# Performance work log

Measured on AMD Instinct MI355X. Metric: run time of the kernel, lower is better.

## Reference

```python
import jax, jax.numpy as jnp
from jax import lax
import numpy as np

T, N, E = 8, 20000, 640000
D_IN, H, K = 2, 64, 3


def setup_inputs() -> dict:
    key = jax.random.key(0)
    ks = jax.random.split(key, 10)
    x = jax.random.normal(ks[0], (T, N, D_IN), dtype=jnp.float32)
    edge_idx = jax.random.randint(ks[1], (T, 2, E), 0, N, dtype=jnp.int64)
    edge_attr = jax.random.uniform(ks[2], (T, E), dtype=jnp.float32)
    Fin = D_IN + H
    s = 0.05
    Wr = jax.random.normal(ks[3], (K, Fin, H), dtype=jnp.float32) * s
    Wu = jax.random.normal(ks[4], (K, Fin, H), dtype=jnp.float32) * s
    Wc = jax.random.normal(ks[5], (K, Fin, H), dtype=jnp.float32) * s
    br = jnp.zeros((H,), dtype=jnp.float32)
    bu = jnp.zeros((H,), dtype=jnp.float32)
    bc = jnp.zeros((H,), dtype=jnp.float32)
    return {"x": x, "edge_idx": edge_idx, "edge_attr": edge_attr,
            "Wr": Wr, "br": br, "Wu": Wu, "bu": bu, "Wc": Wc, "bc": bc}


def reference(x, edge_idx, edge_attr, Wr, br, Wu, bu, Wc, bc):
    n = x.shape[1]
    k_hops = Wr.shape[0]

    def cheb(v, src, dst, wn, W, b):
        # Chebyshev recursion on scaled Laplacian (PyG ChebConv, lambda_max=2)
        def prop(t):
            return jax.ops.segment_sum(wn[:, None] * t[src], dst, num_segments=n)
        Tx0 = v
        out = Tx0 @ W[0]
        Tx1 = prop(Tx0)
        out = out + Tx1 @ W[1]
        for kk in range(2, k_hops):
            Tx2 = 2.0 * prop(Tx1) - Tx0
            out = out + Tx2 @ W[kk]
            Tx0, Tx1 = Tx1, Tx2
        return out + b

    def step(h, inp):
        x_t, ei, w_t = inp
        src, dst = ei[0], ei[1]
        # sym-normalized Laplacian, scaled by 2/lambda_max=1; self-loop weight is 0
        deg = jax.ops.segment_sum(w_t, src, num_segments=n)
        safe = jnp.where(deg > 0, deg, 1.0)
        dinv = jnp.where(deg > 0, lax.rsqrt(safe), 0.0)
        wn = -dinv[src] * w_t * dinv[dst]
        comb = jnp.concatenate([x_t, h], axis=1)
        r = jax.nn.sigmoid(cheb(comb, src, dst, wn, Wr, br))
        u = jax.nn.sigmoid(cheb(comb, src, dst, wn, Wu, bu))
        c = jnp.tanh(cheb(jnp.concatenate([x_t, r * h], axis=1), src, dst, wn, Wc, bc))
        h_new = u * h + (1.0 - u) * c
        return h_new, None

    h0 = jnp.zeros((n, br.shape[0]), dtype=x.dtype)
    h_final, _ = lax.scan(step, h0, (x, edge_idx, edge_attr))
    return h_final
```

## Files before the change

kernel.cpp:

```cpp
#include <hip/hip_runtime.h>

#define NN 20000
#define EE 640000
#define TT 8
#define HF 64
#define AS 232
#define ACS 104
#define BSS 194
#define PBLK 5000
#define TILE 2560
#define NBIN 250
#define BWID 80
#define ECAP 3072
#define LCAP 24

typedef _Float16 f16;
typedef unsigned int uint;
typedef unsigned char uchar;
typedef __attribute__((ext_vector_type(8))) _Float16 half8;
typedef __attribute__((ext_vector_type(4))) float floatx4;
typedef __attribute__((ext_vector_type(4))) uint uint4v;

__device__ __forceinline__ float lo16f(uint v) { return (float)__builtin_bit_cast(f16, (unsigned short)(v & 0xffff)); }
__device__ __forceinline__ float hi16f(uint v) { return (float)__builtin_bit_cast(f16, (unsigned short)(v >> 16)); }
__device__ __forceinline__ uint pk16(float a, float b) {
    unsigned short ua = __builtin_bit_cast(unsigned short, (f16)a);
    unsigned short ub = __builtin_bit_cast(unsigned short, (f16)b);
    return (uint)ua | ((uint)ub << 16);
}

__global__ __launch_bounds__(256) void k_prepW(
    const float* __restrict__ Wr, const float* __restrict__ Wu, const float* __restrict__ Wc,
    f16* __restrict__ Wp, f16* __restrict__ Wcp)
{
    int idx = blockIdx.x * 256 + threadIdx.x;
    if (idx < 8 * 7 * 64) {
        int lane = idx & 63;
        int kb = (idx >> 6) % 7;
        int nb = (idx >> 6) / 7;
        int col = nb * 16 + (lane & 15);
        int g = col >> 6, jj = col & 63;
        const float* W = (g == 0) ? Wr : Wu;
        half8 v;
        #pragma unroll
        for (int e = 0; e < 8; e++) {
            int k = kb * 32 + ((lane >> 4) << 3) + e;
            float val = 0.f;
            if (k < 192)      { int hop = k >> 6; int i = 2 + (k & 63); val = W[(hop * 66 + i) * 64 + jj]; }
            else if (k < 198) { int q = k - 192;  int hop = q >> 1;     val = W[(hop * 66 + (q & 1)) * 64 + jj]; }
            v[e] = (f16)val;
        }
        *(half8*)&Wp[(size_t)idx * 8] = v;
        return;
    }
    int idx2 = idx - 8 * 7 * 64;
    if (idx2 >= 12 * 3 * 64) return;
    int lane = idx2 & 63;
    int kb = (idx2 >> 6) % 3;
    int nbc = (idx2 >> 6) / 3;
    int col = nbc * 16 + (lane & 15);
    int mode = col >> 6, j = col & 63;
    half8 v;
    #pragma unroll
    for (int e = 0; e < 8; e++) {
        int k = kb * 32 + ((lane >> 4) << 3) + e;
        float val = 0.f;
        if (k < 66) {
            if (mode == 0)      val = Wc[(0 * 66 + k) * 64 + j] - Wc[(2 * 66 + k) * 64 + j];
            else if (mode == 1) val = Wc[(1 * 66 + k) * 64 + j];
            else                val = Wc[(2 * 66 + k) * 64 + j];
        }
        v[e] = (f16)val;
    }
    *(half8*)&Wcp[(size_t)idx2 * 8] = v;
}

__global__ __launch_bounds__(256) void k_pack(
    const float* __restrict__ x, uint* __restrict__ xf)
{
    int idx = blockIdx.x * 256 + threadIdx.x;
    if (idx < TT * NN) xf[idx] = pk16(x[2 * idx], x[2 * idx + 1]);
}

__global__ __launch_bounds__(256) void k_bin(
    const int* __restrict__ eidx, const float* __restrict__ eatt,
    int* __restrict__ binptr, uint2* __restrict__ ebuf,
    int* __restrict__ sbinptr, uint* __restrict__ sbuf)
{
    __shared__ uint2 buf[NBIN][LCAP];
    __shared__ uint  sbl[NBIN][LCAP];
    __shared__ int lcnt[NBIN], scnt[NBIN];
    __shared__ int scan[256];
    __shared__ int gb[NBIN];
    int tid = threadIdx.x;
    if (tid < NBIN) { lcnt[tid] = 0; scnt[tid] = 0; }
    __syncthreads();
    int tl = blockIdx.x / 250, tile = blockIdx.x % 250;
    const int*   src = eidx + (size_t)tl * 2 * EE + tile * TILE;
    const int*   dst = src + EE;
    const float* w   = eatt + (size_t)tl * EE + tile * TILE;
    int* bp = binptr + tl * NBIN;
    int* sp = sbinptr + tl * NBIN;
    size_t ebase = (size_t)tl * NBIN * ECAP;
    #pragma unroll
    for (int i = 0; i < TILE / 256; i++) {
        int e = i * 256 + tid;
        int s = __builtin_nontemporal_load(&src[e]);
        int d = __builtin_nontemporal_load(&dst[e]);
        float wv = __builtin_nontemporal_load(&w[e]);
        int bin = d / BWID;
        uint2 ent = make_uint2(((uint)d << 16) | (uint)s, __float_as_uint(wv));
        int p = atomicAdd(&lcnt[bin], 1);
        if (p < LCAP) buf[bin][p] = ent;
        else {
            int gp = atomicAdd(&bp[bin], 1);
            if (gp < ECAP) ebuf[ebase + (size_t)bin * ECAP + gp] = ent;
        }
        int sbin = s / BWID;
        uint sent = (pk16(wv, 0.f) << 16) | (uint)s;
        int sq = atomicAdd(&scnt[sbin], 1);
        if (sq < LCAP) sbl[sbin][sq] = sent;
        else {
            int gp = atomicAdd(&sp[sbin], 1);
            if (gp < ECAP) sbuf[ebase + (size_t)sbin * ECAP + gp] = sent;
        }
    }
    __syncthreads();
    {
        int c = (tid < NBIN) ? (lcnt[tid] < LCAP ? lcnt[tid] : LCAP) : 0;
        scan[tid] = c;
        __syncthreads();
        #pragma unroll
        for (int o = 1; o < 256; o <<= 1) {
            int v = (tid >= o) ? scan[tid - o] : 0;
            __syncthreads();
            scan[tid] += v;
            __syncthreads();
        }
        if (c > 0) gb[tid] = atomicAdd(&bp[tid], c);
        __syncthreads();
        int total = scan[255];
        for (int i = tid; i < total; i += 256) {
            int lo = 0, hi = 255;
            #pragma unroll
            for (int it = 0; it < 8; it++) { int mid = (lo + hi) >> 1; if (scan[mid] > i) hi = mid; else lo = mid + 1; }
            int p = i - (lo ? scan[lo - 1] : 0);
            int gp = gb[lo] + p;
            if (gp < ECAP) ebuf[ebase + (size_t)lo * ECAP + gp] = buf[lo][p];
        }
    }
    __syncthreads();
    {
        int c = (tid < NBIN) ? (scnt[tid] < LCAP ? scnt[tid] : LCAP) : 0;
        scan[tid] = c;
        __syncthreads();
        #pragma unroll
        for (int o = 1; o < 256; o <<= 1) {
            int v = (tid >= o) ? scan[tid - o] : 0;
            __syncthreads();
            scan[tid] += v;
            __syncthreads();
        }
        if (c > 0) gb[tid] = atomicAdd(&sp[tid], c);
        __syncthreads();
        int total = scan[255];
        for (int i = tid; i < total; i += 256) {
            int lo = 0, hi = 255;
            #pragma unroll
            for (int it = 0; it < 8; it++) { int mid = (lo + hi) >> 1; if (scan[mid] > i) hi = mid; else lo = mid + 1; }
            int p = i - (lo ? scan[lo - 1] : 0);
            int gp = gb[lo] + p;
            if (gp < ECAP) sbuf[ebase + (size_t)lo * ECAP + gp] = sbl[lo][p];
        }
    }
}

__global__ __launch_bounds__(256) void k_degred(
    const uint* __restrict__ sbuf, const int* __restrict__ sbinptr,
    float* __restrict__ dinv)
{
    __shared__ float dacc[BWID];
    int tl = blockIdx.x / NBIN, b = blockIdx.x % NBIN, tid = threadIdx.x;
    int nume = sbinptr[tl * NBIN + b]; if (nume > ECAP) nume = ECAP;
    if (tid < BWID) dacc[tid] = 0.f;
    __syncthreads();
    size_t base = (size_t)(tl * NBIN + b) * ECAP;
    for (int i = tid; i < nume; i += 256) {
        uint e = sbuf[base + i];
        atomicAdd(&dacc[(e & 0xffff) - b * BWID], hi16f(e));
    }
    __syncthreads();
    if (tid < BWID) {
        float d = dacc[tid];
        dinv[(size_t)tl * NN + b * BWID + tid] = d > 0.f ? 1.f / sqrtf(d) : 0.f;
    }
}

__global__ __launch_bounds__(256) void k_csr(
    const uint2* __restrict__ ebuf, const int* __restrict__ binptr,
    const float* __restrict__ dinv,
    uint* __restrict__ entries, int* __restrict__ row_ptr, int* __restrict__ cnt)
{
    __shared__ uint proc[ECAP];
    __shared__ uchar lnb[ECAP];
    __shared__ uint staged[ECAP];
    __shared__ int lcnt[BWID], loff[BWID];
    int tl = blockIdx.x / NBIN, b = blockIdx.x % NBIN, tid = threadIdx.x;
    int nume = binptr[tl * NBIN + b]; if (nume > ECAP) nume = ECAP;
    const float* dv = dinv + (size_t)tl * NN;
    size_t base = (size_t)(tl * NBIN + b) * ECAP;
    if (tid < BWID) lcnt[tid] = 0;
    __syncthreads();
    for (int i = tid; i < nume; i += 256) {
        uint2 ent = ebuf[base + i];
        int s = ent.x & 0xffff;
        int d = ent.x >> 16;
        float wv = __uint_as_float(ent.y);
        float wn = -dv[s] * wv * dv[d];
        unsigned short wb = __builtin_bit_cast(unsigned short, (f16)wn);
        proc[i] = ((uint)wb << 16) | (uint)s;
        int ln = d - b * BWID;
        lnb[i] = (uchar)ln;
        atomicAdd(&lcnt[ln], 1);
    }
    __syncthreads();
    if (tid == 0) {
        int run = 0;
        for (int i = 0; i < BWID; i++) { loff[i] = run; run += lcnt[i]; }
    }
    __syncthreads();
    if (tid < BWID) {
        int n = tl * NN + b * BWID + tid;
        row_ptr[n] = (int)base + loff[tid];
        cnt[n] = lcnt[tid];
    }
    __syncthreads();
    for (int i = tid; i < nume; i += 256) {
        int p = atomicAdd(&loff[lnb[i]], 1);
        staged[p] = proc[i];
    }
    __syncthreads();
    for (int i = tid; i < nume; i += 256)
        entries[base + i] = staged[i];
}

__device__ __forceinline__ void gatherq(
    const f16* __restrict__ src_mat, const uint* wnb, int mp, int fg, int grp,
    float acc[8])
{
    #pragma unroll
    for (int k = 0; k < 8; k++) acc[k] = 0.f;
    int e = 0;
    for (; e + 32 <= mp; e += 32) {
        uint ee[4]; uint4v rr[4];
        #pragma unroll
        for (int k = 0; k < 4; k++) ee[k] = wnb[e + 8 * k + grp];
        #pragma unroll
        for (int k = 0; k < 4; k++) rr[k] = *(const uint4v*)&src_mat[(size_t)(ee[k] & 0xffff) * HF + fg * 8];
        #pragma unroll
        for (int k = 0; k < 4; k++) {
            float w = hi16f(ee[k]);
            acc[0] += w * lo16f(rr[k].x); acc[1] += w * hi16f(rr[k].x);
            acc[2] += w * lo16f(rr[k].y); acc[3] += w * hi16f(rr[k].y);
            acc[4] += w * lo16f(rr[k].z); acc[5] += w * hi16f(rr[k].z);
            acc[6] += w * lo16f(rr[k].w); acc[7] += w * hi16f(rr[k].w);
        }
    }
    for (; e < mp; e += 8) {
        uint ent = wnb[e + grp];
        uint4v r = *(const uint4v*)&src_mat[(size_t)(ent & 0xffff) * HF + fg * 8];
        float w = hi16f(ent);
        acc[0] += w * lo16f(r.x); acc[1] += w * hi16f(r.x);
        acc[2] += w * lo16f(r.y); acc[3] += w * hi16f(r.y);
        acc[4] += w * lo16f(r.z); acc[5] += w * hi16f(r.z);
        acc[6] += w * lo16f(r.w); acc[7] += w * hi16f(r.w);
    }
    #pragma unroll
    for (int o = 8; o <= 32; o <<= 1) {
        #pragma unroll
        for (int k = 0; k < 8; k++) acc[k] += __shfl_xor(acc[k], o);
    }
}

__global__ __launch_bounds__(256) void k_prop(
    const f16* __restrict__ src_mat, const f16* __restrict__ base,
    f16* __restrict__ dst,
    const int* __restrict__ row_ptr, const int* __restrict__ cnt,
    const uint* __restrict__ entries,
    float alpha, float beta,
    const uint* __restrict__ xsrc, const uint* __restrict__ xbase,
    uint* __restrict__ xdst)
{
    __shared__ uint wnbuf[4][128];
    int ws = threadIdx.x >> 6, lane = threadIdx.x & 63;
    int node = blockIdx.x * 4 + ws;
    int m = cnt[node]; if (m > 128) m = 128;
    int st = row_ptr[node];
    int mp = (m + 7) & ~7;
    for (int idx = lane; idx < mp; idx += 64)
        wnbuf[ws][idx] = (idx < m) ? entries[st + idx] : 0u;
    asm volatile("s_waitcnt lgkmcnt(0)" ::: "memory");

    int fg = lane & 7, grp = lane >> 3;
    float acc[8];
    gatherq(src_mat, wnbuf[ws], mp, fg, grp, acc);
    if (grp == 0) {
        float r[8];
        #pragma unroll
        for (int k = 0; k < 8; k++) r[k] = alpha * acc[k];
        if (base) {
            uint4v bv = *(const uint4v*)&base[(size_t)node * HF + fg * 8];
            r[0] += beta * lo16f(bv.x); r[1] += beta * hi16f(bv.x);
            r[2] += beta * lo16f(bv.y); r[3] += beta * hi16f(bv.y);
            r[4] += beta * lo16f(bv.z); r[5] += beta * hi16f(bv.z);
            r[6] += beta * lo16f(bv.w); r[7] += beta * hi16f(bv.w);
        }
        uint4v out;
        out.x = pk16(r[0], r[1]); out.y = pk16(r[2], r[3]);
        out.z = pk16(r[4], r[5]); out.w = pk16(r[6], r[7]);
        *(uint4v*)&dst[(size_t)node * HF + fg * 8] = out;
    }

    if (xdst) {
        float xa0 = 0.f, xa1 = 0.f;
        for (int i = lane; i < mp; i += 64) {
            uint ent = wnbuf[ws][i];
            uint xv = xsrc[ent & 0xffff];
            float wn = hi16f(ent);
            xa0 += wn * lo16f(xv);
            xa1 += wn * hi16f(xv);
        }
        #pragma unroll
        for (int o = 32; o >= 1; o >>= 1) {
            xa0 += __shfl_xor(xa0, o);
            xa1 += __shfl_xor(xa1, o);
        }
        if (lane == 0) {
            float r0 = xa0, r1 = xa1;
            r0 *= alpha; r1 *= alpha;
            if (xbase) { uint bv = xbase[node]; r0 += beta * lo16f(bv); r1 += beta * hi16f(bv); }
            xdst[node] = pk16(r0, r1);
        }
    }
}

__global__ __launch_bounds__(256) void k_prop_fin(
    const f16* __restrict__ S, const f16* __restrict__ B0,
    const f16* __restrict__ u, const float* __restrict__ h_in,
    float* __restrict__ h_out, f16* __restrict__ hA_out,
    const int* __restrict__ row_ptr, const int* __restrict__ cnt,
    const uint* __restrict__ entries)
{
    __shared__ uint wnbuf[4][128];
    int ws = threadIdx.x >> 6, lane = threadIdx.x & 63;
    int node = blockIdx.x * 4 + ws;
    int m = cnt[node]; if (m > 128) m = 128;
    int st = row_ptr[node];
    int mp = (m + 7) & ~7;
    for (int idx = lane; idx < mp; idx += 64)
        wnbuf[ws][idx] = (idx < m) ? entries[st + idx] : 0u;
    asm volatile("s_waitcnt lgkmcnt(0)" ::: "memory");

    int fg = lane & 7, grp = lane >> 3;
    float acc[8];
    gatherq(S, wnbuf[ws], mp, fg, grp, acc);
    if (grp == 0) {
        uint4v b0v = *(const uint4v*)&B0[(size_t)node * HF + fg * 8];
        uint4v uv  = *(const uint4v*)&u[(size_t)node * HF + fg * 8];
        float bb[8] = { lo16f(b0v.x), hi16f(b0v.x), lo16f(b0v.y), hi16f(b0v.y),
                        lo16f(b0v.z), hi16f(b0v.z), lo16f(b0v.w), hi16f(b0v.w) };
        float uu[8] = { lo16f(uv.x), hi16f(uv.x), lo16f(uv.y), hi16f(uv.y),
                        lo16f(uv.z), hi16f(uv.z), lo16f(uv.w), hi16f(uv.w) };
        float4 h01 = *(const float4*)&h_in[(size_t)node * HF + fg * 8];
        float4 h23 = *(const float4*)&h_in[(size_t)node * HF + fg * 8 + 4];
        float hp[8] = { h01.x, h01.y, h01.z, h01.w, h23.x, h23.y, h23.z, h23.w };
        float hn[8];
        #pragma unroll
        for (int k = 0; k < 8; k++) {
            float c = tanhf(acc[k] + bb[k]);
            hn[k] = uu[k] * hp[k] + (1.f - uu[k]) * c;
        }
        *(float4*)&h_out[(size_t)node * HF + fg * 8]     = make_float4(hn[0], hn[1], hn[2], hn[3]);
        *(float4*)&h_out[(size_t)node * HF + fg * 8 + 4] = make_float4(hn[4], hn[5], hn[6], hn[7]);
        uint4v ha;
        ha.x = pk16(hn[0], hn[1]); ha.y = pk16(hn[2], hn[3]);
        ha.z = pk16(hn[4], hn[5]); ha.w = pk16(hn[6], hn[7]);
        *(uint4v*)&hA_out[(size_t)node * HF + fg * 8] = ha;
    }
}

#define MFMA16(a, b, c) __builtin_amdgcn_mfma_f32_16x16x32_f16(a, b, c, 0, 0, 0)

__global__ __launch_bounds__(512) void k_ru(
    const f16* __restrict__ hA, const f16* __restrict__ t1, const f16* __restrict__ t2,
    const uint* __restrict__ xf, const uint* __restrict__ t1x, const uint* __restrict__ t2x,
    const f16* __restrict__ Wp, const f16* __restrict__ Wcp,
    const float* __restrict__ br, const float* __restrict__ bu, const float* __restrict__ bc,
    f16* __restrict__ u_out,
    f16* __restrict__ B0, f16* __restrict__ B1, f16* __restrict__ B2)
{
    __shared__ __attribute__((aligned(16))) f16 At[64][AS];
    __shared__ __attribute__((aligned(16))) f16 Ac[64][ACS];
    __shared__ f16 Ub[64][68];
    int n0 = blockIdx.x * 64;
    int tid = threadIdx.x;

    for (int idx = tid; idx < 64 * 8 * 3; idx += 512) {
        int a = idx >> 9, r = (idx >> 3) & 63, s = idx & 7;
        const f16* src = (a == 0) ? hA : (a == 1 ? t1 : t2);
        int gn = n0 + r;
        half8 v = {0, 0, 0, 0, 0, 0, 0, 0};
        if (gn < NN) v = *(const half8*)&src[(size_t)gn * HF + s * 8];
        *(half8*)&At[r][a * 64 + s * 8] = v;
    }
    for (int idx = tid; idx < 64 * 17; idx += 512) {
        int r = idx / 17, c = idx % 17;
        *(uint*)((char*)&At[r][198] + 4 * c) = 0u;
    }
    for (int idx = tid; idx < 64 * 3; idx += 512) {
        int r = idx & 63, a = idx >> 6;
        const uint* src = (a == 0) ? xf : (a == 1 ? t1x : t2x);
        int gn = n0 + r;
        uint v = 0;
        if (gn < NN) v = src[gn];
        *(uint*)&At[r][192 + 2 * a] = v;
    }
    for (int idx = tid; idx < 64; idx += 512) {
        int gn = n0 + idx;
        *(uint*)&Ac[idx][0] = (gn < NN) ? xf[gn] : 0u;
    }
    for (int idx = tid; idx < 64 * 15; idx += 512) {
        int r = idx / 15, c = idx % 15;
        *(uint*)((char*)&Ac[r][66] + 4 * c) = 0u;
    }
    __syncthreads();

    int wid = tid >> 6, lane = tid & 63;
    int mrow = (wid & 1) * 32;
    int nb0 = (wid >> 1) * 2;
    int arow = mrow + (lane & 15);
    int koff = (lane >> 4) << 3;
    floatx4 z = {0.f, 0.f, 0.f, 0.f};
    {
        floatx4 acc00 = z, acc01 = z, acc10 = z, acc11 = z;
        #pragma unroll
        for (int kb = 0; kb < 7; kb++) {
            half8 a0 = *(const half8*)&At[arow][kb * 32 + koff];
            half8 a1 = *(const half8*)&At[arow + 16][kb * 32 + koff];
            half8 b0 = *(const half8*)&Wp[(size_t)(((nb0    ) * 7 + kb) * 64 + lane) * 8];
            half8 b1 = *(const half8*)&Wp[(size_t)(((nb0 + 1) * 7 + kb) * 64 + lane) * 8];
            acc00 = MFMA16(a0, b0, acc00);
            acc10 = MFMA16(a1, b0, acc10);
            acc01 = MFMA16(a0, b1, acc01);
            acc11 = MFMA16(a1, b1, acc11);
        }
        bool isR = nb0 < 4;
        #pragma unroll
        for (int mi = 0; mi < 2; mi++) {
            #pragma unroll
            for (int ni = 0; ni < 2; ni++) {
                floatx4 a = (mi == 0) ? (ni == 0 ? acc00 : acc01) : (ni == 0 ? acc10 : acc11);
                int jj = ((nb0 + ni) * 16 + (lane & 15)) & 63;
                float bias = isR ? br[jj] : bu[jj];
                int rbase = mrow + mi * 16 + ((lane >> 4) << 2);
                #pragma unroll
                for (int e = 0; e < 4; e++) {
                    int rloc = rbase + e;
                    float s = 1.f / (1.f + __expf(-(a[e] + bias)));
                    if (isR) {
                        float hv = (float)At[rloc][jj];
                        Ac[rloc][2 + jj] = (f16)(s * hv);
                    } else {
                        Ub[rloc][jj] = (f16)s;
                    }
                }
            }
        }
    }
    __syncthreads();

    for (int idx = tid; idx < 64 * 32; idx += 512) {
        int n = idx >> 5, c = idx & 31;
        int gn = n0 + n;
        if (gn < NN) *(uint*)&u_out[(size_t)gn * HF + 2 * c] = *(uint*)&Ub[n][2 * c];
    }
    f16* Bs = &At[0][0];
    #pragma unroll
    for (int i = 0; i < 6; i++) {
        int t = wid * 6 + i;
        int nbc = t >> 2, mq = t & 3;
        int ar = mq * 16 + (lane & 15);
        floatx4 acc;
        float binit = (nbc < 4) ? bc[nbc * 16 + (lane & 15)] : 0.f;
        acc[0] = binit; acc[1] = binit; acc[2] = binit; acc[3] = binit;
        #pragma unroll
        for (int kb = 0; kb < 3; kb++) {
            half8 a = *(const half8*)&Ac[ar][kb * 32 + koff];
            half8 b = *(const half8*)&Wcp[(size_t)(((nbc * 3 + kb) * 64) + lane) * 8];
            acc = MFMA16(a, b, acc);
        }
        int rbase = mq * 16 + ((lane >> 4) << 2);
        int col = nbc * 16 + (lane & 15);
        #pragma unroll
        for (int e = 0; e < 4; e++)
            Bs[(size_t)(rbase + e) * BSS + col] = (f16)acc[e];
    }
    __syncthreads();

    for (int idx = tid; idx < 64 * 96; idx += 512) {
        int n = idx / 96, c = idx % 96;
        int gn = n0 + n;
        if (gn < NN) {
            int col = 2 * c;
            f16* Bdst = (col < 64) ? B0 : (col < 128 ? B1 : B2);
            *(uint*)&Bdst[(size_t)gn * HF + (col & 63)] = *(uint*)&Bs[(size_t)n * BSS + col];
        }
    }
}


extern "C" void kernel_launch(void* const* d_in, const int* in_sizes, int n_in,
                              void* d_out, int out_size, void* d_ws, size_t ws_size,
                              hipStream_t stream)
{
    const float* x    = (const float*)d_in[0];
    const int*   eidx = (const int*)d_in[1];
    const float* eatt = (const float*)d_in[2];
    const float* Wr   = (const float*)d_in[3];
    const float* br   = (const float*)d_in[4];
    const float* Wu   = (const float*)d_in[5];
    const float* bu   = (const float*)d_in[6];
    const float* Wc   = (const float*)d_in[7];
    const float* bc   = (const float*)d_in[8];

    char* ws = (char*)d_ws;
    size_t off = 0;
    auto alloc = [&](size_t bytes) -> void* {
        void* p = ws + off;
        off += (bytes + 255) & ~(size_t)255;
        return p;
    };
    const size_t FB = (size_t)NN * HF * 2;
    float* h_f32   = (float*)alloc((size_t)NN * HF * 4);
    f16*   hA      = (f16*)alloc(FB);
    f16*   t1      = (f16*)alloc(FB);
    f16*   t2      = (f16*)alloc(FB);
    f16*   u       = (f16*)alloc(FB);
    f16*   B0      = (f16*)alloc(FB);
    f16*   B1      = (f16*)alloc(FB);
    f16*   B2      = (f16*)alloc(FB);
    float* dinv    = (float*)alloc((size_t)TT * NN * 4);
    uint*  xf      = (uint*)alloc((size_t)TT * NN * 4);
    uint*  t1x     = (uint*)alloc((size_t)NN * 4);
    uint*  t2x     = (uint*)alloc((size_t)NN * 4);
    int*   bptr2   = (int*)alloc((size_t)2 * TT * NBIN * 4);
    uint2* ebuf    = (uint2*)alloc((size_t)TT * NBIN * ECAP * 8);
    uint*  sbuf    = (uint*)alloc((size_t)TT * NBIN * ECAP * 4);
    uint*  entr    = (uint*)alloc((size_t)TT * NBIN * ECAP * 4);
    int*   rowp    = (int*)alloc((size_t)TT * NN * 4);
    int*   cnt     = (int*)alloc((size_t)TT * NN * 4);
    f16*   Wp      = (f16*)alloc((size_t)8 * 7 * 64 * 8 * 2);
    f16*   Wcp     = (f16*)alloc((size_t)12 * 3 * 64 * 8 * 2);
    int* binptr = bptr2;
    int* sbinptr = bptr2 + TT * NBIN;

    hipMemsetAsync(h_f32, 0, (size_t)NN * HF * 4 + FB, stream);
    hipMemsetAsync(bptr2, 0, (size_t)2 * TT * NBIN * 4, stream);
    k_prepW<<<30, 256, 0, stream>>>(Wr, Wu, Wc, Wp, Wcp);
    k_pack <<<(TT * NN + 255) / 256, 256, 0, stream>>>(x, xf);

    k_bin   <<<TT * 250, 256, 0, stream>>>(eidx, eatt, binptr, ebuf, sbinptr, sbuf);
    k_degred<<<TT * NBIN, 256, 0, stream>>>(sbuf, sbinptr, dinv);
    k_csr   <<<TT * NBIN, 256, 0, stream>>>(ebuf, binptr, dinv, entr, rowp, cnt);

    const int GB = (NN + 63) / 64;

    for (int t = 0; t < TT; ++t) {
        const int* rp = rowp + (size_t)t * NN;
        const int* cp = cnt + (size_t)t * NN;
        uint* xft = xf + (size_t)t * NN;

        k_prop<<<PBLK, 256, 0, stream>>>(hA, nullptr, t1, rp, cp, entr, 1.f,  0.f, xft, nullptr, t1x);
        k_prop<<<PBLK, 256, 0, stream>>>(t1, hA,      t2, rp, cp, entr, 2.f, -1.f, t1x, xft,     t2x);

        k_ru<<<GB, 512, 0, stream>>>(hA, t1, t2, xft, t1x, t2x, Wp, Wcp,
                                     br, bu, bc, u, B0, B1, B2);

        k_prop<<<PBLK, 256, 0, stream>>>(B2, B1, t2, rp, cp, entr, 2.f, 1.f, nullptr, nullptr, nullptr);

        float* hdst = (t == TT - 1) ? (float*)d_out : h_f32;
        k_prop_fin<<<PBLK, 256, 0, stream>>>(t2, B0, u, h_f32, hdst, hA, rp, cp, entr);
    }
}
```

Measured before the change: 721.4 us.

## Fuse second Chebyshev propagation into the gate GEMM kernel

```diff
diff --git a/kernel.cpp b/kernel.cpp
--- a/kernel.cpp
+++ b/kernel.cpp
@@ -28,6 +28,8 @@
     unsigned short ub = __builtin_bit_cast(unsigned short, (f16)b);
     return (uint)ua | ((uint)ub << 16);
 }
+
+#define MFMA16(a, b, c) __builtin_amdgcn_mfma_f32_16x16x32_f16(a, b, c, 0, 0, 0)
 
 __global__ __launch_bounds__(256) void k_prepW(
     const float* __restrict__ Wr, const float* __restrict__ Wu, const float* __restrict__ Wc,
@@ -336,8 +338,7 @@
             xa1 += __shfl_xor(xa1, o);
         }
         if (lane == 0) {
-            float r0 = xa0, r1 = xa1;
-            r0 *= alpha; r1 *= alpha;
+            float r0 = alpha * xa0, r1 = alpha * xa1;
             if (xbase) { uint bv = xbase[node]; r0 += beta * lo16f(bv); r1 += beta * hi16f(bv); }
             xdst[node] = pk16(r0, r1);
         }
@@ -389,59 +390,104 @@
     }
 }
 
-#define MFMA16(a, b, c) __builtin_amdgcn_mfma_f32_16x16x32_f16(a, b, c, 0, 0, 0)
-
-__global__ __launch_bounds__(512) void k_ru(
-    const f16* __restrict__ hA, const f16* __restrict__ t1, const f16* __restrict__ t2,
-    const uint* __restrict__ xf, const uint* __restrict__ t1x, const uint* __restrict__ t2x,
+__global__ __launch_bounds__(256) void k_rug(
+    const f16* __restrict__ hA, const f16* __restrict__ t1,
+    const uint* __restrict__ xf, const uint* __restrict__ t1x,
     const f16* __restrict__ Wp, const f16* __restrict__ Wcp,
     const float* __restrict__ br, const float* __restrict__ bu, const float* __restrict__ bc,
+    const int* __restrict__ row_ptr, const int* __restrict__ cnt, const uint* __restrict__ entries,
     f16* __restrict__ u_out,
     f16* __restrict__ B0, f16* __restrict__ B1, f16* __restrict__ B2)
 {
     __shared__ __attribute__((aligned(16))) f16 At[64][AS];
     __shared__ __attribute__((aligned(16))) f16 Ac[64][ACS];
     __shared__ f16 Ub[64][68];
+    __shared__ uint wn4[4][128];
     int n0 = blockIdx.x * 64;
     int tid = threadIdx.x;
 
-    for (int idx = tid; idx < 64 * 8 * 3; idx += 512) {
+    for (int idx = tid; idx < 64 * 8 * 2; idx += 256) {
         int a = idx >> 9, r = (idx >> 3) & 63, s = idx & 7;
-        const f16* src = (a == 0) ? hA : (a == 1 ? t1 : t2);
+        const f16* src = a ? t1 : hA;
         int gn = n0 + r;
         half8 v = {0, 0, 0, 0, 0, 0, 0, 0};
         if (gn < NN) v = *(const half8*)&src[(size_t)gn * HF + s * 8];
         *(half8*)&At[r][a * 64 + s * 8] = v;
     }
-    for (int idx = tid; idx < 64 * 17; idx += 512) {
+    for (int idx = tid; idx < 64 * 17; idx += 256) {
         int r = idx / 17, c = idx % 17;
         *(uint*)((char*)&At[r][198] + 4 * c) = 0u;
     }
-    for (int idx = tid; idx < 64 * 3; idx += 512) {
+    for (int idx = tid; idx < 64 * 2; idx += 256) {
         int r = idx & 63, a = idx >> 6;
-        const uint* src = (a == 0) ? xf : (a == 1 ? t1x : t2x);
+        const uint* src = a ? t1x : xf;
         int gn = n0 + r;
         uint v = 0;
         if (gn < NN) v = src[gn];
         *(uint*)&At[r][192 + 2 * a] = v;
     }
-    for (int idx = tid; idx < 64; idx += 512) {
+    for (int idx = tid; idx < 64; idx += 256) {
         int gn = n0 + idx;
         *(uint*)&Ac[idx][0] = (gn < NN) ? xf[gn] : 0u;
     }
-    for (int idx = tid; idx < 64 * 15; idx += 512) {
+    for (int idx = tid; idx < 64 * 15; idx += 256) {
         int r = idx / 15, c = idx % 15;
         *(uint*)((char*)&Ac[r][66] + 4 * c) = 0u;
     }
     __syncthreads();
 
     int wid = tid >> 6, lane = tid & 63;
-    int mrow = (wid & 1) * 32;
-    int nb0 = (wid >> 1) * 2;
-    int arow = mrow + (lane & 15);
+    int fg = lane & 7, grp = lane >> 3;
+
+    for (int i = 0; i < 16; i++) {
+        int r = wid * 16 + i;
+        int node = n0 + r;
+        int m = 0, st = 0;
+        if (node < NN) { m = cnt[node]; if (m > 128) m = 128; st = row_ptr[node]; }
+        int mp = (m + 7) & ~7;
+        for (int idx = lane; idx < mp; idx += 64)
+            wn4[wid][idx] = (idx < m) ? entries[st + idx] : 0u;
+        asm volatile("s_waitcnt lgkmcnt(0)" ::: "memory");
+        float acc[8];
+        gatherq(t1, wn4[wid], mp, fg, grp, acc);
+        if (grp == 0) {
+            half8 h0 = *(const half8*)&At[r][fg * 8];
+            float v[8];
+            #pragma unroll
+            for (int k = 0; k < 8; k++) v[k] = 2.f * acc[k] - (float)h0[k];
+            uint4v o;
+            o.x = pk16(v[0], v[1]); o.y = pk16(v[2], v[3]);
+            o.z = pk16(v[4], v[5]); o.w = pk16(v[6], v[7]);
+            *(uint4v*)&At[r][128 + fg * 8] = o;
+        }
+        float xa0 = 0.f, xa1 = 0.f;
+        for (int ii = lane; ii < mp; ii += 64) {
+            uint ent = wn4[wid][ii];
+            uint xv = t1x[ent & 0xffff];
+            float wn = hi16f(ent);
+            xa0 += wn * lo16f(xv);
+            xa1 += wn * hi16f(xv);
+        }
+        #pragma unroll
+        for (int o = 32; o >= 1; o >>= 1) {
+            xa0 += __shfl_xor(xa0, o);
+            xa1 += __shfl_xor(xa1, o);
+        }
+        if (lane == 0) {
+            uint xb = (node < NN) ? xf[node] : 0u;
+            *(uint*)&At[r][196] = pk16(2.f * xa0 - lo16f(xb), 2.f * xa1 - hi16f(xb));
+        }
+    }
+    __syncthreads();
+
     int koff = (lane >> 4) << 3;
     floatx4 z = {0.f, 0.f, 0.f, 0.f};
-    {
+    #pragma unroll
+    for (int sub = 0; sub < 2; sub++) {
+        int vw = (wid << 1) | sub;
+        int mrow = (vw & 1) * 32;
+        int nb0 = (vw >> 1) * 2;
+        int arow = mrow + (lane & 15);
         floatx4 acc00 = z, acc01 = z, acc10 = z, acc11 = z;
         #pragma unroll
         for (int kb = 0; kb < 7; kb++) {
@@ -479,16 +525,16 @@
     }
     __syncthreads();
 
-    for (int idx = tid; idx < 64 * 32; idx += 512) {
+    for (int idx = tid; idx < 64 * 32; idx += 256) {
         int n = idx >> 5, c = idx & 31;
         int gn = n0 + n;
         if (gn < NN) *(uint*)&u_out[(size_t)gn * HF + 2 * c] = *(uint*)&Ub[n][2 * c];
     }
     f16* Bs = &At[0][0];
     #pragma unroll
-    for (int i = 0; i < 6; i++) {
-        int t = wid * 6 + i;
-        int nbc = t >> 2, mq = t & 3;
+    for (int i = 0; i < 12; i++) {
+        int tt = wid * 12 + i;
+        int nbc = tt >> 2, mq = tt & 3;
         int ar = mq * 16 + (lane & 15);
         floatx4 acc;
         float binit = (nbc < 4) ? bc[nbc * 16 + (lane & 15)] : 0.f;
@@ -507,7 +553,7 @@
     }
     __syncthreads();
 
-    for (int idx = tid; idx < 64 * 96; idx += 512) {
+    for (int idx = tid; idx < 64 * 96; idx += 256) {
         int n = idx / 96, c = idx % 96;
         int gn = n0 + n;
         if (gn < NN) {
@@ -552,7 +598,6 @@
     float* dinv    = (float*)alloc((size_t)TT * NN * 4);
     uint*  xf      = (uint*)alloc((size_t)TT * NN * 4);
     uint*  t1x     = (uint*)alloc((size_t)NN * 4);
-    uint*  t2x     = (uint*)alloc((size_t)NN * 4);
     int*   bptr2   = (int*)alloc((size_t)2 * TT * NBIN * 4);
     uint2* ebuf    = (uint2*)alloc((size_t)TT * NBIN * ECAP * 8);
     uint*  sbuf    = (uint*)alloc((size_t)TT * NBIN * ECAP * 4);
@@ -580,11 +625,10 @@
         const int* cp = cnt + (size_t)t * NN;
         uint* xft = xf + (size_t)t * NN;
 
-        k_prop<<<PBLK, 256, 0, stream>>>(hA, nullptr, t1, rp, cp, entr, 1.f,  0.f, xft, nullptr, t1x);
-        k_prop<<<PBLK, 256, 0, stream>>>(t1, hA,      t2, rp, cp, entr, 2.f, -1.f, t1x, xft,     t2x);
-
-        k_ru<<<GB, 512, 0, stream>>>(hA, t1, t2, xft, t1x, t2x, Wp, Wcp,
-                                     br, bu, bc, u, B0, B1, B2);
+        k_prop<<<PBLK, 256, 0, stream>>>(hA, nullptr, t1, rp, cp, entr, 1.f, 0.f, xft, nullptr, t1x);
+
+        k_rug<<<GB, 256, 0, stream>>>(hA, t1, xft, t1x, Wp, Wcp, br, bu, bc,
+                                      rp, cp, entr, u, B0, B1, B2);
 
         k_prop<<<PBLK, 256, 0, stream>>>(B2, B1, t2, rp, cp, entr, 2.f, 1.f, nullptr, nullptr, nullptr);
 
```

Result: slower. 934.4 us (+29.5%).
